# Kernel optimization log

Measured on AMD Instinct MI355X. Metric: run time of the kernel, lower is better.

The kernel has to match this reference:

```python
import jax, jax.numpy as jnp
from jax import lax
import numpy as np

# ---- module hyperparameters (from init_kwargs) ----
INPUT_SIZE = 448
RF_MIN = 2
ECC_SLOPE = 0.2
DEG2PX = 30
FOVEA_SIZE = 4.0
RF_QUANT = 1.0
STRIDE = 2
OUT_SIZE = (INPUT_SIZE + 1) // STRIDE  # 224


def _build_masks_and_rfs():
    """Replicates CenterDependentPool2D._build (numpy, static)."""
    out = OUT_SIZE
    center = out // 2
    ecc = round(FOVEA_SIZE * DEG2PX / 2)
    ecc_step = round(RF_QUANT * DEG2PX / 2)
    fovea_px = FOVEA_SIZE * DEG2PX
    yy, xx = np.mgrid[0:out, 0:out]
    d2 = (yy - center) ** 2 + (xx - center) ** 2

    def disk(r):  # skimage.draw.disk uses strict < radius
        return (d2 < r * r).astype(np.float32)

    masks, rfs = [], []
    if ecc > out / 2:
        masks.append(np.ones((out, out), np.float32))
        rfs.append(RF_MIN)
    else:
        masks.append(disk(ecc))
        rfs.append(RF_MIN)
        ecc += ecc_step
        while ecc < out / 2:
            masks.append(disk(ecc) - disk(ecc - ecc_step))  # annulus
            rfs.append(RF_MIN + round(ECC_SLOPE * (ecc * 2 - fovea_px)))
            ecc += ecc_step
        masks.append(1.0 - disk(ecc - ecc_step))  # outer ring
        rfs.append(RF_MIN + round(ECC_SLOPE * (ecc * 2 - fovea_px)))
    return [jnp.asarray(m) for m in masks], rfs


_MASKS, _RFS = _build_masks_and_rfs()


def setup_inputs() -> dict:
    key = jax.random.key(0)
    x = jax.random.normal(key, (8, 64, INPUT_SIZE, INPUT_SIZE), dtype=jnp.float32)
    return {"x": x}


def reference(x) -> jnp.ndarray:
    neg_inf = jnp.asarray(-jnp.inf, x.dtype)
    out = jnp.zeros(x.shape[:2] + (OUT_SIZE, OUT_SIZE), x.dtype)
    for mask, rf in zip(_MASKS, _RFS):
        k = max(rf, 1)
        pad_lo = (k - 1) // 2          # floor((k-1)/2)
        pad_hi = (k - 1) - pad_lo      # ceil((k-1)/2)
        xp = jnp.pad(x, ((0, 0), (0, 0), (pad_lo, pad_hi), (pad_lo, pad_hi)), mode="reflect")
        pooled = lax.reduce_window(
            xp, neg_inf, lax.max,
            window_dimensions=(1, 1, k, k),
            window_strides=(1, 1, STRIDE, STRIDE),
            padding="VALID",
        )  # (B, C, OUT_SIZE, OUT_SIZE)
        out = out + pooled * mask
    return out
```

## Files before the change

kernel.cpp:

```cpp
#include <hip/hip_runtime.h>
#include <climits>


#define IN_SZ 448
#define OUT_SZ 224
#define CENTER 112
#define TILE_X 32
#define TILE_Y 16
#define TSTR 92
#define NTHREADS 256

__device__ __forceinline__ int reflect448(int g) {
    g = (g < 0) ? -g : g;
    g = (g >= IN_SZ) ? (2 * IN_SZ - 2 - g) : g;
    return g;
}

__device__ __forceinline__ int ring_k(int d2) {
    if (d2 < 3600)  return 2;
    if (d2 < 5625)  return 8;
    if (d2 < 8100)  return 14;
    if (d2 < 11025) return 20;
    return 26;
}

__device__ __forceinline__ int isqrt_floor(int v) {
    int s = (int)sqrtf((float)v);
    if (s > 0 && s * s > v) --s;
    if ((s + 1) * (s + 1) <= v) ++s;
    return s;
}

__device__ __forceinline__ float4 max4(float4 a, float4 b) {
    return make_float4(fmaxf(a.x, b.x), fmaxf(a.y, b.y),
                       fmaxf(a.z, b.z), fmaxf(a.w, b.w));
}

template <int K, int O>
__device__ __forceinline__ void ring_pass(
    const float* __restrict__ T, float* __restrict__ H, float* __restrict__ VP,
    float* __restrict__ op, int tid, int lyA, int lyB, int ox0, int oy0)
{
    constexpr int KH = K / 2;
    constexpr int S  = O & 3;
    constexpr int NF = S + K + 6;
    constexpr int R  = (NF + 3) >> 2;
    constexpr int B0 = (O - S) >> 2;

    const int rows  = lyB - lyA + 1;
    const int nh    = 2 * (rows - 1) + K;
    const int nv    = rows - 1 + KH;
    const int tbase = 2 * lyA + O;

    for (int t = tid; t < nh * 8; t += NTHREADS) {
        const int hr = t >> 3, g = t & 7;
        const float4* trow = (const float4*)&T[(tbase + hr) * TSTR];
        float f[4 * R];
#pragma unroll
        for (int q = 0; q < R; ++q)
            *(float4*)&f[4 * q] = trow[2 * g + B0 + q];
        float p[KH + 3];
#pragma unroll
        for (int j = 0; j < KH + 3; ++j)
            p[j] = fmaxf(f[S + 2 * j], f[S + 2 * j + 1]);
        float4 W;
        if constexpr (KH == 1) {
            W = make_float4(p[0], p[1], p[2], p[3]);
        } else {
            float core = p[3];
#pragma unroll
            for (int j = 4; j < KH; ++j) core = fmaxf(core, p[j]);
            W.x = fmaxf(fmaxf(p[0], p[1]), fmaxf(p[2], core));
            W.y = fmaxf(fmaxf(p[1], p[2]), fmaxf(core, p[KH]));
            W.z = fmaxf(fmaxf(p[2], core), fmaxf(p[KH], p[KH + 1]));
            W.w = fmaxf(fmaxf(core, p[KH]), fmaxf(p[KH + 1], p[KH + 2]));
        }
        *(float4*)&H[hr * 32 + 4 * g] = W;
    }
    __syncthreads();

    for (int t = tid; t < nv * 8; t += NTHREADS) {
        const int v = t >> 3, g = t & 7;
        float4 a = *(const float4*)&H[(2 * v) * 32 + 4 * g];
        float4 b = *(const float4*)&H[(2 * v + 1) * 32 + 4 * g];
        *(float4*)&VP[v * 32 + 4 * g] = max4(a, b);
    }
    __syncthreads();

    for (int t = tid; t < rows * 8; t += NTHREADS) {
        const int lr = t >> 3, g = t & 7;
        float4 m = *(const float4*)&VP[lr * 32 + 4 * g];
#pragma unroll
        for (int j = 1; j < KH; ++j)
            m = max4(m, *(const float4*)&VP[(lr + j) * 32 + 4 * g]);
        const int oy  = oy0 + lyA + lr;
        const int dy2 = (oy - CENTER) * (oy - CENTER);
        const int oxb = ox0 + 4 * g;
        float* orow = op + (size_t)oy * OUT_SZ + oxb;
        const float mv[4] = {m.x, m.y, m.z, m.w};
#pragma unroll
        for (int e = 0; e < 4; ++e) {
            const int dx = oxb + e - CENTER;
            if (ring_k(dy2 + dx * dx) == K) orow[e] = mv[e];
        }
    }
}

template <int KMAX>
__device__ __forceinline__ void run_rings(
    const float* T, float* H, float* VP, float* op, int tid,
    const int* lyA, const int* lyB, int ox0, int oy0)
{
    if (lyA[0] <= lyB[0])
        ring_pass<2, (KMAX - 2) / 2>(T, H, VP, op, tid, lyA[0], lyB[0], ox0, oy0);
    if constexpr (KMAX >= 8)
        if (lyA[1] <= lyB[1])
            ring_pass<8, (KMAX - 8) / 2>(T, H, VP, op, tid, lyA[1], lyB[1], ox0, oy0);
    if constexpr (KMAX >= 14)
        if (lyA[2] <= lyB[2])
            ring_pass<14, (KMAX - 14) / 2>(T, H, VP, op, tid, lyA[2], lyB[2], ox0, oy0);
    if constexpr (KMAX >= 20)
        if (lyA[3] <= lyB[3])
            ring_pass<20, (KMAX - 20) / 2>(T, H, VP, op, tid, lyA[3], lyB[3], ox0, oy0);
    if constexpr (KMAX >= 26)
        if (lyA[4] <= lyB[4])
            ring_pass<26, 0>(T, H, VP, op, tid, lyA[4], lyB[4], ox0, oy0);
}

__global__ __launch_bounds__(NTHREADS, 4)
void CenterDependentPool2D_kernel(const float* __restrict__ x,
                                  float* __restrict__ out)
{
    __shared__ float T[56 * TSTR];
    __shared__ float H[56 * 32];
    __shared__ float VP[28 * 32];

    const int tid = threadIdx.x;
    const int ox0 = blockIdx.x * TILE_X;
    const int oy0 = blockIdx.y * TILE_Y;
    const int plane = blockIdx.z;

    const float* __restrict__ in = x + (size_t)plane * IN_SZ * IN_SZ;
    float* __restrict__ op = out + (size_t)plane * OUT_SZ * OUT_SZ;

    const int a = ox0 - CENTER, b = ox0 + TILE_X - 1 - CENTER;
    int xmn2, xmx2;
    if (a > 0)      { xmn2 = a * a; xmx2 = b * b; }
    else if (b < 0) { xmn2 = b * b; xmx2 = a * a; }
    else            { xmn2 = 0; const int m = (-a > b) ? -a : b; xmx2 = m * m; }

    const int R2a[5] = {0, 3600, 5625, 8100, 11025};
    const int R2b[5] = {3600, 5625, 8100, 11025, INT_MAX};
    const int KS[5]  = {2, 8, 14, 20, 26};

    int lyA[5], lyB[5];
    int kmax = 2;
    const int d0 = oy0 - CENTER;
#pragma unroll
    for (int i = 0; i < 5; ++i) {
        int A = 1, B = 0;
        int shi;
        bool nonempty;
        if (i == 4) { shi = 1000; nonempty = true; }
        else {
            const int hi2 = R2b[i] - 1 - xmn2;
            nonempty = (hi2 >= 0);
            shi = nonempty ? isqrt_floor(hi2) : 0;
        }
        if (nonempty) {
            const int lo2 = R2a[i] - xmx2;
            const int slo = (lo2 <= 0) ? 0 : isqrt_floor(lo2 - 1) + 1;
            if (d0 >= 0) { A = slo - d0; B = shi - d0; }
            else         { const int dp = -d0; A = dp - shi; B = dp - slo; }
            A = A < 0 ? 0 : A;
            B = B > TILE_Y - 1 ? TILE_Y - 1 : B;
        }
        lyA[i] = A; lyB[i] = B;
        if (A <= B) kmax = KS[i];
    }

    const int plt    = (kmax - 1) >> 1;
    const int span_x = 2 * (TILE_X - 1) + kmax;
    const int span_y = 2 * (TILE_Y - 1) + kmax;
    const int x_org  = 2 * ox0 - plt;
    const int y_org  = 2 * oy0 - plt;
    const int gpr    = (span_x + 3) >> 2;
    const int ntT    = span_y * gpr;

    const bool fast = (x_org >= 0) && ((x_org & 3) == 0) &&
                      (x_org + 4 * gpr <= IN_SZ) &&
                      (y_org >= 0) && (y_org + span_y <= IN_SZ);
    if (fast) {
        for (int t = tid; t < ntT; t += NTHREADS) {
            const int r = t / gpr, c = t - r * gpr;
            const float4 v =
                *(const float4*)(in + (size_t)(y_org + r) * IN_SZ + x_org + 4 * c);
            *(float4*)&T[r * TSTR + 4 * c] = v;
        }
    } else {
        for (int t = tid; t < ntT; t += NTHREADS) {
            const int r = t / gpr, c4 = (t - r * gpr) * 4;
            const float* rowp = in + (size_t)reflect448(y_org + r) * IN_SZ;
            float4 v;
            v.x = rowp[reflect448(x_org + c4 + 0)];
            v.y = rowp[reflect448(x_org + c4 + 1)];
            v.z = rowp[reflect448(x_org + c4 + 2)];
            v.w = rowp[reflect448(x_org + c4 + 3)];
            *(float4*)&T[r * TSTR + c4] = v;
        }
    }
    __syncthreads();

    switch (kmax) {
        case 2:  run_rings<2 >(T, H, VP, op, tid, lyA, lyB, ox0, oy0); break;
        case 8:  run_rings<8 >(T, H, VP, op, tid, lyA, lyB, ox0, oy0); break;
        case 14: run_rings<14>(T, H, VP, op, tid, lyA, lyB, ox0, oy0); break;
        case 20: run_rings<20>(T, H, VP, op, tid, lyA, lyB, ox0, oy0); break;
        default: run_rings<26>(T, H, VP, op, tid, lyA, lyB, ox0, oy0); break;
    }
}

extern "C" void kernel_launch(void* const* d_in, const int* in_sizes, int n_in,
                              void* d_out, int out_size, void* d_ws, size_t ws_size,
                              hipStream_t stream) {
    const float* x = (const float*)d_in[0];
    float* out = (float*)d_out;
    dim3 grid(OUT_SZ / TILE_X, OUT_SZ / TILE_Y, 8 * 64);
    dim3 block(NTHREADS, 1, 1);
    hipLaunchKernelGGL(CenterDependentPool2D_kernel, grid, block, 0, stream, x, out);
}
```

Measured before the change: 764.7 us.

## Reorder separable max to vertical-first, shrink tile rows, always load full halo

Each ring pass now reduces vertical row pairs first across the full tile width, then does the horizontal window on the half-height buffer, which halves the number of horizontal-window rows. TILE_Y drops from 16 to 14 and launch bounds go from 4 to 5 blocks per CU to raise occupancy. The per-tile kmax specialisation is replaced by a fixed 26-wide halo load with a per-element reflect fallback. This drops the template switch but loads a larger halo for foveal tiles.

```diff
diff --git a/kernel.cpp b/kernel.cpp
--- a/kernel.cpp
+++ b/kernel.cpp
@@ -6,9 +6,15 @@
 #define OUT_SZ 224
 #define CENTER 112
 #define TILE_X 32
-#define TILE_Y 16
+#define TILE_Y 14
 #define TSTR 92
+#define VSTR 92
+#define HSTR 32
 #define NTHREADS 256
+
+#define T_ROWS 52
+#define V_ROWS 26
+#define GPRC 22
 
 __device__ __forceinline__ int reflect448(int g) {
     g = (g < 0) ? -g : g;
@@ -36,29 +42,40 @@
                        fmaxf(a.z, b.z), fmaxf(a.w, b.w));
 }
 
-template <int K, int O>
+template <int K>
 __device__ __forceinline__ void ring_pass(
-    const float* __restrict__ T, float* __restrict__ H, float* __restrict__ VP,
-    float* __restrict__ op, int tid, int lyA, int lyB, int ox0, int oy0)
+    const float* __restrict__ T, float* __restrict__ VPT,
+    float* __restrict__ HW, float* __restrict__ op,
+    int tid, int lyA, int lyB, int ox0, int oy0)
 {
+    constexpr int O  = (26 - K) / 2;
     constexpr int KH = K / 2;
     constexpr int S  = O & 3;
     constexpr int NF = S + K + 6;
     constexpr int R  = (NF + 3) >> 2;
     constexpr int B0 = (O - S) >> 2;
+    constexpr int CGN = (GPRC - B0 < 14 + R) ? (GPRC - B0) : (14 + R);
 
     const int rows  = lyB - lyA + 1;
-    const int nh    = 2 * (rows - 1) + K;
     const int nv    = rows - 1 + KH;
     const int tbase = 2 * lyA + O;
 
-    for (int t = tid; t < nh * 8; t += NTHREADS) {
-        const int hr = t >> 3, g = t & 7;
-        const float4* trow = (const float4*)&T[(tbase + hr) * TSTR];
+    for (int t = tid; t < nv * CGN; t += NTHREADS) {
+        const int v = t / CGN, c = B0 + (t - v * CGN);
+        const float* r0 = &T[(tbase + 2 * v) * TSTR + 4 * c];
+        const float4 a = *(const float4*)r0;
+        const float4 b = *(const float4*)(r0 + TSTR);
+        *(float4*)&VPT[v * VSTR + 4 * c] = max4(a, b);
+    }
+    __syncthreads();
+
+    for (int t = tid; t < nv * 8; t += NTHREADS) {
+        const int v = t >> 3, g = t & 7;
+        const float4* vrow = (const float4*)&VPT[v * VSTR];
         float f[4 * R];
 #pragma unroll
         for (int q = 0; q < R; ++q)
-            *(float4*)&f[4 * q] = trow[2 * g + B0 + q];
+            *(float4*)&f[4 * q] = vrow[2 * g + B0 + q];
         float p[KH + 3];
 #pragma unroll
         for (int j = 0; j < KH + 3; ++j)
@@ -75,24 +92,16 @@
             W.z = fmaxf(fmaxf(p[2], core), fmaxf(p[KH], p[KH + 1]));
             W.w = fmaxf(fmaxf(core, p[KH]), fmaxf(p[KH + 1], p[KH + 2]));
         }
-        *(float4*)&H[hr * 32 + 4 * g] = W;
-    }
-    __syncthreads();
-
-    for (int t = tid; t < nv * 8; t += NTHREADS) {
-        const int v = t >> 3, g = t & 7;
-        float4 a = *(const float4*)&H[(2 * v) * 32 + 4 * g];
-        float4 b = *(const float4*)&H[(2 * v + 1) * 32 + 4 * g];
-        *(float4*)&VP[v * 32 + 4 * g] = max4(a, b);
+        *(float4*)&HW[v * HSTR + 4 * g] = W;
     }
     __syncthreads();
 
     for (int t = tid; t < rows * 8; t += NTHREADS) {
         const int lr = t >> 3, g = t & 7;
-        float4 m = *(const float4*)&VP[lr * 32 + 4 * g];
+        float4 m = *(const float4*)&HW[lr * HSTR + 4 * g];
 #pragma unroll
         for (int j = 1; j < KH; ++j)
-            m = max4(m, *(const float4*)&VP[(lr + j) * 32 + 4 * g]);
+            m = max4(m, *(const float4*)&HW[(lr + j) * HSTR + 4 * g]);
         const int oy  = oy0 + lyA + lr;
         const int dy2 = (oy - CENTER) * (oy - CENTER);
         const int oxb = ox0 + 4 * g;
@@ -106,34 +115,13 @@
     }
 }
 
-template <int KMAX>
-__device__ __forceinline__ void run_rings(
-    const float* T, float* H, float* VP, float* op, int tid,
-    const int* lyA, const int* lyB, int ox0, int oy0)
-{
-    if (lyA[0] <= lyB[0])
-        ring_pass<2, (KMAX - 2) / 2>(T, H, VP, op, tid, lyA[0], lyB[0], ox0, oy0);
-    if constexpr (KMAX >= 8)
-        if (lyA[1] <= lyB[1])
-            ring_pass<8, (KMAX - 8) / 2>(T, H, VP, op, tid, lyA[1], lyB[1], ox0, oy0);
-    if constexpr (KMAX >= 14)
-        if (lyA[2] <= lyB[2])
-            ring_pass<14, (KMAX - 14) / 2>(T, H, VP, op, tid, lyA[2], lyB[2], ox0, oy0);
-    if constexpr (KMAX >= 20)
-        if (lyA[3] <= lyB[3])
-            ring_pass<20, (KMAX - 20) / 2>(T, H, VP, op, tid, lyA[3], lyB[3], ox0, oy0);
-    if constexpr (KMAX >= 26)
-        if (lyA[4] <= lyB[4])
-            ring_pass<26, 0>(T, H, VP, op, tid, lyA[4], lyB[4], ox0, oy0);
-}
-
-__global__ __launch_bounds__(NTHREADS, 4)
+__global__ __launch_bounds__(NTHREADS, 5)
 void CenterDependentPool2D_kernel(const float* __restrict__ x,
                                   float* __restrict__ out)
 {
-    __shared__ float T[56 * TSTR];
-    __shared__ float H[56 * 32];
-    __shared__ float VP[28 * 32];
+    __shared__ float T[T_ROWS * TSTR];
+    __shared__ float VPT[V_ROWS * VSTR];
+    __shared__ float HW[V_ROWS * HSTR];
 
     const int tid = threadIdx.x;
     const int ox0 = blockIdx.x * TILE_X;
@@ -151,10 +139,8 @@
 
     const int R2a[5] = {0, 3600, 5625, 8100, 11025};
     const int R2b[5] = {3600, 5625, 8100, 11025, INT_MAX};
-    const int KS[5]  = {2, 8, 14, 20, 26};
 
     int lyA[5], lyB[5];
-    int kmax = 2;
     const int d0 = oy0 - CENTER;
 #pragma unroll
     for (int i = 0; i < 5; ++i) {
@@ -176,48 +162,32 @@
             B = B > TILE_Y - 1 ? TILE_Y - 1 : B;
         }
         lyA[i] = A; lyB[i] = B;
-        if (A <= B) kmax = KS[i];
-    }
-
-    const int plt    = (kmax - 1) >> 1;
-    const int span_x = 2 * (TILE_X - 1) + kmax;
-    const int span_y = 2 * (TILE_Y - 1) + kmax;
-    const int x_org  = 2 * ox0 - plt;
-    const int y_org  = 2 * oy0 - plt;
-    const int gpr    = (span_x + 3) >> 2;
-    const int ntT    = span_y * gpr;
-
-    const bool fast = (x_org >= 0) && ((x_org & 3) == 0) &&
-                      (x_org + 4 * gpr <= IN_SZ) &&
-                      (y_org >= 0) && (y_org + span_y <= IN_SZ);
-    if (fast) {
-        for (int t = tid; t < ntT; t += NTHREADS) {
-            const int r = t / gpr, c = t - r * gpr;
-            const float4 v =
-                *(const float4*)(in + (size_t)(y_org + r) * IN_SZ + x_org + 4 * c);
-            *(float4*)&T[r * TSTR + 4 * c] = v;
-        }
-    } else {
-        for (int t = tid; t < ntT; t += NTHREADS) {
-            const int r = t / gpr, c4 = (t - r * gpr) * 4;
-            const float* rowp = in + (size_t)reflect448(y_org + r) * IN_SZ;
-            float4 v;
-            v.x = rowp[reflect448(x_org + c4 + 0)];
-            v.y = rowp[reflect448(x_org + c4 + 1)];
-            v.z = rowp[reflect448(x_org + c4 + 2)];
-            v.w = rowp[reflect448(x_org + c4 + 3)];
-            *(float4*)&T[r * TSTR + c4] = v;
-        }
+    }
+
+    const int x_org = 2 * ox0 - 12;
+    const int y_org = 2 * oy0 - 12;
+    for (int t = tid; t < T_ROWS * GPRC; t += NTHREADS) {
+        const int r = t / GPRC, c4 = (t - r * GPRC) * 4;
+        const int gy = y_org + r, gx = x_org + c4;
+        float4 v;
+        if ((unsigned)gy < IN_SZ && (unsigned)gx <= IN_SZ - 4) {
+            v = *(const float4*)(in + (size_t)gy * IN_SZ + gx);
+        } else {
+            const float* rowp = in + (size_t)reflect448(gy) * IN_SZ;
+            v.x = rowp[reflect448(gx + 0)];
+            v.y = rowp[reflect448(gx + 1)];
+            v.z = rowp[reflect448(gx + 2)];
+            v.w = rowp[reflect448(gx + 3)];
+        }
+        *(float4*)&T[r * TSTR + c4] = v;
     }
     __syncthreads();
 
-    switch (kmax) {
-        case 2:  run_rings<2 >(T, H, VP, op, tid, lyA, lyB, ox0, oy0); break;
-        case 8:  run_rings<8 >(T, H, VP, op, tid, lyA, lyB, ox0, oy0); break;
-        case 14: run_rings<14>(T, H, VP, op, tid, lyA, lyB, ox0, oy0); break;
-        case 20: run_rings<20>(T, H, VP, op, tid, lyA, lyB, ox0, oy0); break;
-        default: run_rings<26>(T, H, VP, op, tid, lyA, lyB, ox0, oy0); break;
-    }
+    if (lyA[0] <= lyB[0]) ring_pass<2 >(T, VPT, HW, op, tid, lyA[0], lyB[0], ox0, oy0);
+    if (lyA[1] <= lyB[1]) ring_pass<8 >(T, VPT, HW, op, tid, lyA[1], lyB[1], ox0, oy0);
+    if (lyA[2] <= lyB[2]) ring_pass<14>(T, VPT, HW, op, tid, lyA[2], lyB[2], ox0, oy0);
+    if (lyA[3] <= lyB[3]) ring_pass<20>(T, VPT, HW, op, tid, lyA[3], lyB[3], ox0, oy0);
+    if (lyA[4] <= lyB[4]) ring_pass<26>(T, VPT, HW, op, tid, lyA[4], lyB[4], ox0, oy0);
 }
 
 extern "C" void kernel_launch(void* const* d_in, const int* in_sizes, int n_in,
```

New measurement: 835.4 us. 1.09x slower.
